# Kernel tuning notes

Measured on AMD Instinct MI355X. Metric: run time of the kernel, lower is better.

The kernel has to match this reference:

```python
import jax, jax.numpy as jnp
import numpy as np
from itertools import product

N_CODONS = 2
ORDER = 2
N_STATES = 25          # calc_number_of_states() with nCodons=2
ALPHA6 = 6             # alphabet_size + 2
OFFSET = 8 + 3 * N_CODONS       # 14, first insert state
TERM1 = OFFSET + 3 * (N_CODONS + 1)  # 23, terminal_1 state

CODE = {'A': [0], 'C': [1], 'G': [2], 'T': [3], 'N': [0, 1, 2, 3], 'X': [5]}


def _state_entries(state, emissions, x_must_preceed):
    ems = ['N'] * (ORDER - len(emissions) + 1) + list(emissions)[-(ORDER + 1):]
    allowed = [[state]]
    for i, e in enumerate(ems):
        allowed.append(CODE[e] + ([4] if i < ORDER - x_must_preceed else []))
    out = []
    for x in product(*allowed):
        found, ok = False, True
        for i in range(1, ORDER + 1):
            if found and x[i] == 4:
                ok = False
                break
            if x[i] != 4:
                found = True
        if ok:
            out.append(x)
    return out


def _emission_index_spec():
    entries, k = [], 0
    def add(state, ems, xp, trainable=True):
        nonlocal k
        ids = _state_entries(state, ems, xp)
        for t, x in enumerate(ids):
            entries.append((x, k + t if trainable else -1))
        if trainable:
            k += len(ids)
    add(0, 'N', 0); add(1, 'A', 0); add(2, 'AT', 0); add(3, 'ATG', 0, False)
    add(4, 'ATGN', 0); add(5, 'ATGNN', 0)
    for s in range(6, 6 + N_CODONS * 3 - 2):
        add(s, 'N', 0)
    add(4 + 3 * N_CODONS, 'T', ORDER)
    add(5 + 3 * N_CODONS, 'TA', ORDER); add(5 + 3 * N_CODONS, 'TG', ORDER)
    add(6 + 3 * N_CODONS, 'TAA', ORDER, False)
    add(6 + 3 * N_CODONS, 'TAG', ORDER, False)
    add(6 + 3 * N_CODONS, 'TGA', ORDER, False)
    add(7 + 3 * N_CODONS, 'N', ORDER)
    for s in range(8 + 3 * N_CODONS, 8 + 3 * N_CODONS + 3 * (N_CODONS + 1)):
        add(s, 'N', 0)
    for i in range(1, ORDER + 1):
        add(TERM1, 'X' * i, ORDER)
    add(TERM1 + 1, 'X' * (ORDER + 1), ORDER, False)
    idx = np.array([e[0] for e in entries], dtype=np.int32)
    widx = np.array([e[1] for e in entries], dtype=np.int32)
    return idx, widx

EM_IDX, EM_WIDX = _emission_index_spec()


def build_A(w):
    # sparse transition structure -> row-softmax over nonzeros -> dense [25,25]
    idx, vals = [], []
    def add(i, j, v):
        idx.append((i, j)); vals.append(v)
    n, k = N_CODONS, 0
    add(0, 0, 1 - w[k]); add(0, 1, w[k]); k += 1
    add(1, 2, 1.0); add(2, 3, 1.0)
    for i in range(n):
        add(3 + 3 * i, 4 + 3 * i, w[k + i])
    k += n
    for i in range(n):
        add(4 + 3 * i, 5 + 3 * i, 1.0)
    for i in range(n):
        add(5 + 3 * i, 6 + 3 * i, 1.0)
    for i in range(n + 1):
        add(3 + 3 * i, OFFSET + 3 * i, w[k + i])
    k += n + 1
    add(3 + 3 * n, 4 + 3 * n, 1 - w[k - 1])
    for i in range(n + 1):
        add(OFFSET + 3 * i, OFFSET + 1 + 3 * i, 1.0)
    for i in range(n + 1):
        add(OFFSET + 1 + 3 * i, OFFSET + 2 + 3 * i, 1.0)
    for i in range(n + 1):
        add(OFFSET + 2 + 3 * i, 4 + 3 * i, w[k + i])
    for i in range(n + 1):
        add(OFFSET + 2 + 3 * i, OFFSET + 3 * i, 1 - w[k + i])
    k += n + 1
    i_del = [3 + 3 * i for i in range(n) for _ in range(n - i)]
    j_del = [4 + 3 * j for i in range(1, n + 1) for j in range(i, n + 1)]
    for i, j in zip(i_del, j_del):
        add(i, j, 1 - w[k] * w[k] ** ((j - i) // 3))
    k += 1
    add(4 + 3 * n, 5 + 3 * n, 1.0); add(5 + 3 * n, 6 + 3 * n, 1.0)
    add(6 + 3 * n, 7 + 3 * n, 1.0)
    add(7 + 3 * n, 7 + 3 * n, 1.0); add(7 + 3 * n, TERM1, 1.0)
    add(TERM1, TERM1, 1.0); add(TERM1, TERM1 + 1, 1.0)
    add(TERM1 + 1, TERM1 + 1, 1.0)
    rows = np.array([i for i, _ in idx]); cols = np.array([j for _, j in idx])
    logits = jnp.stack([jnp.asarray(v, jnp.float32) for v in vals])
    M = jnp.full((N_STATES, N_STATES), -jnp.inf, jnp.float32).at[rows, cols].set(logits)
    A = jax.nn.softmax(M, axis=-1)
    return jnp.where(jnp.isfinite(M), A, 0.0)


def build_B(w):
    # sparse emission values (trainable weights or fixed 1), per-state softmax over nonzeros
    vals = jnp.where(EM_WIDX >= 0, w[np.clip(EM_WIDX, 0, None)], 1.0)
    rows = EM_IDX[:, 0]
    flat = EM_IDX[:, 1] * 36 + EM_IDX[:, 2] * 6 + EM_IDX[:, 3]
    M = jnp.full((N_STATES, ALPHA6 ** 3), -jnp.inf, jnp.float32).at[rows, flat].set(vals)
    B = jax.nn.softmax(M, axis=-1)
    return jnp.where(jnp.isfinite(M), B, 0.0)  # [25, 216]


def build_I(w):
    n_init = 3 + 3 * N_CODONS  # states 0..8 get initial mass
    p = jax.nn.softmax(w[:n_init])
    return jnp.zeros((N_STATES,), jnp.float32).at[:n_init].set(p)


def _forward(transition_kernel, emission_kernel, init_kernel, tokens):
    A = build_A(transition_kernel)
    Bf = build_B(emission_kernel)
    I = build_I(init_kernel)
    Bt, T = tokens.shape
    pad = jnp.full((Bt, ORDER), 4, tokens.dtype)  # '4' = no preceding emission
    tp = jnp.concatenate([pad, tokens], axis=1)
    flat = tp[:, :-2] * 36 + tp[:, 1:-1] * 6 + tp[:, 2:]  # [Bt, T]
    E = jnp.moveaxis(Bf.T[flat], 1, 0)  # [T, Bt, 25]
    alpha = I[None, :] * E[0]
    s = alpha.sum(-1, keepdims=True)
    alpha = alpha / s
    ll = jnp.log(s[..., 0])
    def step(carry, e):
        a, ll = carry
        a = (a @ A) * e
        s = a.sum(-1, keepdims=True)
        return (a / s, ll + jnp.log(s[..., 0])), None
    (alpha, ll), _ = jax.lax.scan(step, (alpha, ll), E[1:])
    return ll  # [Bt] per-sequence log-likelihood


def setup_inputs() -> dict:
    key = jax.random.key(0)
    k1, k2, k3, k4 = jax.random.split(key, 4)
    return {
        'transition_kernel': jax.random.normal(k1, (10,), jnp.float32) * 0.05,
        'emission_kernel': jax.random.normal(k2, (5400,), jnp.float32) * 0.05,
        'init_kernel': jax.random.normal(k3, (25,), jnp.float32) * 0.05,
        'tokens': jax.random.randint(k4, (512, 2048), 0, 4, jnp.int32),
    }


def reference(transition_kernel, emission_kernel, init_kernel, tokens):
    return _forward(transition_kernel, emission_kernel, init_kernel, tokens)
```

## Files before the change

### kernel.cpp

```cpp
#include <hip/hip_runtime.h>
#include <hip/hip_bf16.h>
#include <math.h>


typedef float v2f __attribute__((ext_vector_type(2)));
typedef float v4f __attribute__((ext_vector_type(4)));

#define NSTATES 25
#define NLIVE   23
#define NFLAT   216
#define NPACK   100
#define TLEN    2048
#define NSEQ    512
#define CHUNKS  16
#define CLEN    128

#define LOG16 2.772588722239781f

__device__ __constant__ int PERMC[24] = {1,4,2,5,3,6,7,10,8,11,9,12,
                                         14,17,15,18,16,19,20,0,21,13,22,23};
__device__ __constant__ int POSA[NLIVE] = {19,0,2,4,1,3,5,6,8,10,7,9,11,21,
                                           12,14,16,13,15,17,18,20,22};

struct WMap { short m[NSTATES * NFLAT]; };

constexpr WMap make_wmap() {
  WMap w{};
  for (int i = 0; i < NSTATES * NFLAT; i++) w.m[i] = -2;
  const unsigned char ST[29] = {0,1,2,3,4,5,6,7,8,9,10,11,11,12,12,12,13,
                                14,15,16,17,18,19,20,21,22,23,23,24};
  const unsigned char M1[29] = {0x1F,0x1F,0x1F,0x11,0x18,0x14,0x1F,0x1F,0x1F,
                                0x1F,0x0F,0x0F,0x0F,0x08,0x08,0x08,0x0F,
                                0x1F,0x1F,0x1F,0x1F,0x1F,0x1F,0x1F,0x1F,0x1F,
                                0x0F,0x0F,0x20};
  const unsigned char M2[29] = {0x1F,0x1F,0x11,0x18,0x14,0x1F,0x1F,0x1F,0x1F,
                                0x1F,0x0F,0x08,0x08,0x01,0x01,0x04,0x0F,
                                0x1F,0x1F,0x1F,0x1F,0x1F,0x1F,0x1F,0x1F,0x1F,
                                0x0F,0x20,0x20};
  const unsigned char M3[29] = {0x0F,0x01,0x08,0x04,0x0F,0x0F,0x0F,0x0F,0x0F,
                                0x0F,0x08,0x01,0x04,0x01,0x04,0x01,0x0F,
                                0x0F,0x0F,0x0F,0x0F,0x0F,0x0F,0x0F,0x0F,0x0F,
                                0x20,0x20,0x20};
  const unsigned char TR[29] = {1,1,1,0,1,1,1,1,1,1,1,1,1,0,0,0,1,
                                1,1,1,1,1,1,1,1,1,1,1,0};
  int k = 0;
  for (int s = 0; s < 29; s++) {
    for (int c1 = 0; c1 < 6; c1++) {
      if (!((M1[s] >> c1) & 1)) continue;
      for (int c2 = 0; c2 < 6; c2++) {
        if (!((M2[s] >> c2) & 1)) continue;
        if (c1 != 4 && c2 == 4) continue;
        for (int c3 = 0; c3 < 6; c3++) {
          if (!((M3[s] >> c3) & 1)) continue;
          w.m[ST[s] * NFLAT + c1 * 36 + c2 * 6 + c3] =
              TR[s] ? (short)(k++) : (short)-1;
        }
      }
    }
  }
  return w;
}
__device__ __constant__ WMap WMAP = make_wmap();

__device__ __forceinline__ unsigned short f2bf(float x) {
  unsigned int u = __float_as_uint(x);
  u += 0x7fffu + ((u >> 16) & 1u);
  return (unsigned short)(u >> 16);
}

struct Wp {
  v2f w01, wA, wB, wC, wD, wE, wF;
  float w4, w5, w8, w11;
};

__device__ __forceinline__ void step_pk(v2f (&Q)[12], const v4f (&F)[6],
                                        const Wp& W) {
  float a0 = Q[9].y,  a3 = Q[2].x,  a6 = Q[2].y,  a9 = Q[5].x;
  float a12 = Q[5].y, a13 = Q[10].y, a16 = Q[8].x, a19 = Q[8].y, a22 = Q[11].x;
  float q9x = Q[9].x, q10x = Q[10].x;

  v2f t01 = a0 * W.w01;
  v2f t44 = a3 * W.wA + a16 * W.wB;
  v2f t77 = a6 * W.wC + a19 * W.wD;
  float n7  = fmaf(a3, W.w4, t77.x);
  v2f tAA = a9 * W.wE + a22 * W.wF;
  float n10 = fmaf(a3, W.w5, fmaf(a6, W.w8, tAA.x));
  float n13 = fmaf(a13, W.w11, a12);

  v2f nQ1 = Q[0] * __builtin_shufflevector(F[0], F[0], 2, 3);
  v2f nQ2 = Q[1] * __builtin_shufflevector(F[1], F[1], 0, 1);
  v2f nQ4 = Q[3] * __builtin_shufflevector(F[2], F[2], 0, 1);
  v2f nQ5 = Q[4] * __builtin_shufflevector(F[2], F[2], 2, 3);
  v2f nQ7 = Q[6] * __builtin_shufflevector(F[3], F[3], 2, 3);
  v2f nQ8 = Q[7] * __builtin_shufflevector(F[4], F[4], 0, 1);

  Q[0]  = (v2f){ t01.y * F[0].x, t44.x * F[0].y };
  Q[3]  = (v2f){ n7    * F[1].z, n10   * F[1].w };
  Q[6]  = (v2f){ t44.y * F[3].x, t77.y * F[3].y };
  Q[9]  = (v2f){ tAA.y * F[4].z, t01.x * F[4].w };
  Q[10] = (v2f){ q9x   * F[5].x, n13   * F[5].y };
  Q[11].x = q10x * F[5].z;
  Q[1] = nQ1; Q[2] = nQ2; Q[4] = nQ4; Q[5] = nQ5; Q[7] = nQ7; Q[8] = nQ8;
}

__device__ __forceinline__ void renorm_pk(v2f (&Q)[12], float& L) {
  v2f acc = ((Q[0] + Q[1]) + (Q[2] + Q[3])) + ((Q[4] + Q[5]) + (Q[6] + Q[7]))
          + ((Q[8] + Q[9]) + (Q[10] + Q[11]));
  float s = acc.x + acc.y;
  if (s > 0.0f) {
    L += __logf(s);
    float r = __fdividef(1.0f, s);
    #pragma unroll
    for (int k = 0; k < 12; k++) Q[k] *= r;
  } else {
    L = -3.0e38f;
  }
}

#define LDROW(F, nt_) { int nt = (nt_); \
  const v4f* er = (const v4f*)(sBt + (((c12 << 2) + nt) << 5)); \
  F[0] = er[0]; F[1] = er[1]; F[2] = er[2]; \
  F[3] = er[3]; F[4] = er[4]; F[5] = er[5]; \
  c12 = p2 * 5 + nt; p2 = nt; }
#define LDSTEP(Fn, Fc, nt_) { LDROW(Fn, nt_); step_pk(Q, Fc, W); }

__global__ __launch_bounds__(512)
void hmm_kernel(const float* __restrict__ wT, const float* __restrict__ wE,
                const float* __restrict__ wI, const int* __restrict__ tokens,
                float* __restrict__ out) {
  __shared__ __align__(16) float          sBt[NPACK * 32];
  __shared__ __align__(16) unsigned short sT[CHUNKS * NLIVE * 24];
  __shared__ float sL[CHUNKS * NLIVE];
  __shared__ float sAW[24];
  __shared__ float sI[32];

  const int tid   = threadIdx.x;
  const int seq   = blockIdx.x;
  const int chunk = tid >> 5;
  const int row   = tid & 31;
  const int* trow = tokens + (size_t)seq * TLEN;

  for (int st = chunk; st < NLIVE; st += 16) {
    const int pos = POSA[st];
    float part = 0.0f;
    for (int c = row; c < NFLAT; c += 32) {
      short m = WMAP.m[st * NFLAT + c];
      if (m == -1) part += expf(1.0f);
      else if (m >= 0) part += expf(wE[m]);
    }
    #pragma unroll
    for (int m = 1; m < 32; m <<= 1) part += __shfl_xor(part, m, 32);
    float inv = 16.0f / part;
    for (int i = row; i < NPACK; i += 32) {
      int c12 = i >> 2, nt = i & 3;
      int p1 = c12 / 5, p2v = c12 - 5 * p1;
      int flat = p1 * 36 + p2v * 6 + nt;
      short m = WMAP.m[st * NFLAT + flat];
      float v = 0.0f;
      if (m == -1) v = expf(1.0f);
      else if (m >= 0) v = expf(wE[m]);
      sBt[i * 32 + pos] = v * inv;
    }
  }
  for (int i = tid; i < NPACK; i += 512) sBt[i * 32 + 23] = 0.0f;
  if (tid == 480) {
    const float w0 = wT[0], w1 = wT[1], w2 = wT[2], w3 = wT[3], w4 = wT[4];
    const float w5 = wT[5], w6 = wT[6], w7 = wT[7], w8 = wT[8], w9 = wT[9];
    { float e0 = expf(1.0f - w0), e1 = expf(w0), is = 1.0f / (e0 + e1);
      sAW[0] = e0 * is; sAW[1] = e1 * is; }
    { float e4 = expf(w1), e14 = expf(w3);
      float e7 = expf(1.0f - w9 * w9), e10 = expf(1.0f - w9 * w9 * w9);
      float is = 1.0f / (e4 + e14 + e7 + e10);
      sAW[2] = e4 * is;  sAW[3] = e14 * is;
      sAW[4] = e7 * is;  sAW[5] = e10 * is; }
    { float e7 = expf(w2), e17 = expf(w4), e10 = expf(1.0f - w9 * w9);
      float is = 1.0f / (e7 + e17 + e10);
      sAW[6] = e7 * is; sAW[7] = e17 * is; sAW[8] = e10 * is; }
    { float e20 = expf(w5), e10 = expf(1.0f - w5), is = 1.0f / (e20 + e10);
      sAW[9] = e20 * is; sAW[10] = e10 * is; }
    sAW[11] = 0.5f; sAW[12] = 0.5f;
    { float e4 = expf(w6), e14 = expf(1.0f - w6), is = 1.0f / (e4 + e14);
      sAW[13] = e4 * is; sAW[14] = e14 * is; }
    { float e7 = expf(w7), e17 = expf(1.0f - w7), is = 1.0f / (e7 + e17);
      sAW[15] = e7 * is; sAW[16] = e17 * is; }
    { float e10 = expf(w8), e20 = expf(1.0f - w8), is = 1.0f / (e10 + e20);
      sAW[17] = e10 * is; sAW[18] = e20 * is; }
    sAW[19] = 0.5f; sAW[20] = 0.5f;
  } else if (tid == 481) {
    float e[9], s = 0.0f;
    for (int i = 0; i < 9; i++) { e[i] = expf(wI[i]); s += e[i]; }
    float inv = 1.0f / s;
    for (int i = 0; i < 9; i++) sI[i] = e[i] * inv;
    for (int i = 9; i < 32; i++) sI[i] = 0.0f;
  }
  __syncthreads();

  float w[21];
  #pragma unroll
  for (int i = 0; i < 21; i++)
    w[i] = __uint_as_float(
        (unsigned)__builtin_amdgcn_readfirstlane(__float_as_uint(sAW[i])));
  Wp W;
  W.w01 = (v2f){w[0],  w[1]};
  W.wA  = (v2f){w[2],  w[3]};
  W.wB  = (v2f){w[13], w[14]};
  W.wC  = (v2f){w[6],  w[7]};
  W.wD  = (v2f){w[15], w[16]};
  W.wE  = (v2f){w[10], w[9]};
  W.wF  = (v2f){w[17], w[18]};
  W.w4 = w[4]; W.w5 = w[5]; W.w8 = w[8]; W.w11 = w[11];

  const int t0 = chunk * CLEN;

  v2f Q[12];
  #pragma unroll
  for (int k = 0; k < 12; k++) {
    Q[k].x = (row == PERMC[2 * k]) ? 1.0f : 0.0f;
    Q[k].y = (row == PERMC[2 * k + 1]) ? 1.0f : 0.0f;
  }
  float L = 0.0f;

  v4f FA[6], FB[6];
  int c12, p2;
  int4 q0 = *(const int4*)(trow + t0);
  int4 q1 = *(const int4*)(trow + t0 + 4);

  int b = 0;
  if (chunk == 0) {
    c12 = 20 + q0.x; p2 = q0.x;
    LDROW(FA, q0.y);
    LDSTEP(FB, FA, q0.z);
    LDSTEP(FA, FB, q0.w);
    LDSTEP(FB, FA, q1.x);
    LDSTEP(FA, FB, q1.y);
    LDSTEP(FB, FA, q1.z);
    LDSTEP(FA, FB, q1.w);
    step_pk(Q, FA, W);
    b = 1;
    q0 = *(const int4*)(trow + 8);
    q1 = *(const int4*)(trow + 12);
  } else {
    int2 pp = *(const int2*)(trow + t0 - 2);
    c12 = pp.x * 5 + pp.y; p2 = pp.y;
  }

  for (; b < CLEN / 8; b++) {
    int4 n0 = q0, n1 = q1;
    if (b + 1 < CLEN / 8) {
      n0 = *(const int4*)(trow + t0 + (b + 1) * 8);
      n1 = *(const int4*)(trow + t0 + (b + 1) * 8 + 4);
    }
    LDROW(FA, q0.x);
    LDSTEP(FB, FA, q0.y);
    LDSTEP(FA, FB, q0.z);
    LDSTEP(FB, FA, q0.w);
    LDSTEP(FA, FB, q1.x);
    LDSTEP(FB, FA, q1.y);
    LDSTEP(FA, FB, q1.z);
    LDSTEP(FB, FA, q1.w);
    step_pk(Q, FB, W);
    if (b & 1) renorm_pk(Q, L);
    q0 = n0; q1 = n1;
  }

  if (L > -1.0e38f) L -= (chunk == 0 ? 127.0f : 128.0f) * LOG16;

  if (row < NLIVE) {
    const int base = (chunk * NLIVE + row) * 24;
    #pragma unroll
    for (int k = 0; k < 12; k++) {
      ushort2 p; p.x = f2bf(Q[k].x); p.y = f2bf(Q[k].y);
      *(ushort2*)&sT[base + 2 * k] = p;
    }
    sL[chunk * NLIVE + row] = L;
  }
  __syncthreads();

  if (tid < 64) {
    const int lane = tid;
    const bool act = (lane < NLIVE);

    int jp = 23;
    #pragma unroll
    for (int pos = 0; pos < 23; pos++)
      if (PERMC[pos] == lane) jp = pos;

    const int tok0 = trow[0];
    const int idx0 = 96 + tok0;

    float v = act ? sI[lane] * sBt[idx0 * 32 + jp] : 0.0f;
    float s = v;
    #pragma unroll
    for (int m = 1; m < 32; m <<= 1) s += __shfl_xor(s, m, 32);
    float ll = __logf(s) - LOG16;
    v = act ? v * __fdividef(1.0f, s) : 0.0f;

    for (int c = 0; c < CHUNKS; c++) {
      float Lj  = act ? sL[c * NLIVE + lane] : -3.0e38f;
      float key = (act && v > 0.0f) ? Lj : -3.0e38f;
      float mx = key;
      #pragma unroll
      for (int m = 1; m < 32; m <<= 1) mx = fmaxf(mx, __shfl_xor(mx, m, 32));
      float wgt = (act && v > 0.0f) ? v * __expf(Lj - mx) : 0.0f;

      float nv = 0.0f;
      #pragma unroll
      for (int r = 0; r < NLIVE; r++) {
        float wr = __shfl(wgt, r, 64);
        nv += wr * __uint_as_float(((unsigned)sT[(c * NLIVE + r) * 24 + jp]) << 16);
      }
      float nva = act ? nv : 0.0f;
      float s2 = nva;
      #pragma unroll
      for (int m = 1; m < 32; m <<= 1) s2 += __shfl_xor(s2, m, 32);
      ll += mx + __logf(s2);
      v = act ? nv * __fdividef(1.0f, s2) : 0.0f;
    }

    if (lane == 0) out[seq] = ll;
  }
}

extern "C" void kernel_launch(void* const* d_in, const int* in_sizes, int n_in,
                              void* d_out, int out_size, void* d_ws, size_t ws_size,
                              hipStream_t stream) {
  const float* wT = (const float*)d_in[0];
  const float* wE = (const float*)d_in[1];
  const float* wI = (const float*)d_in[2];
  const int* tokens = (const int*)d_in[3];
  float* out = (float*)d_out;
  (void)d_ws; (void)ws_size;

  hmm_kernel<<<NSEQ, 512, 0, stream>>>(wT, wE, wI, tokens, out);
}
```

Baseline: 120.9 us.

## Precompute emission table once and stream rows via scalar loads per wavefront

Moves the per-block emission table construction into a separate prep kernel that writes a compact global table, removing redundant exp work from every block. The main loop now fetches each emission row with s_load_dwordx8 into scalar registers, using readfirstlane'd tokens and software double-buffering, instead of LDS vector reads. Blocks grow to 1024 threads with one 64-lane wave per chunk. Risks include scalar-cache latency on the serial dependency chain, half-idle 64-wide waves (only 23 lanes live), and the extra kernel launch.

Measured after the change: 148.6 us. 22.9% more time.

```diff
diff --git a/kernel.cpp b/kernel.cpp
--- a/kernel.cpp
+++ b/kernel.cpp
@@ -4,7 +4,7 @@
 
 
 typedef float v2f __attribute__((ext_vector_type(2)));
-typedef float v4f __attribute__((ext_vector_type(4)));
+typedef float v8f __attribute__((ext_vector_type(8)));
 
 #define NSTATES 25
 #define NLIVE   23
@@ -17,10 +17,16 @@
 
 #define LOG16 2.772588722239781f
 
+#define RFL(x) __builtin_amdgcn_readfirstlane(x)
+
 __device__ __constant__ int PERMC[24] = {1,4,2,5,3,6,7,10,8,11,9,12,
                                          14,17,15,18,16,19,20,0,21,13,22,23};
 __device__ __constant__ int POSA[NLIVE] = {19,0,2,4,1,3,5,6,8,10,7,9,11,21,
                                            12,14,16,13,15,17,18,20,22};
+__device__ __constant__ int SLOTP[24] = {12,13,0,1,2,3,14,15,4,5,6,7,
+                                         16,17,8,9,10,11,18,19,20,21,22,23};
+
+__device__ __align__(16) float gBt[NPACK * 24];
 
 struct WMap { short m[NSTATES * NFLAT]; };
 
@@ -73,8 +79,9 @@
   float w4, w5, w8, w11;
 };
 
-__device__ __forceinline__ void step_pk(v2f (&Q)[12], const v4f (&F)[6],
-                                        const Wp& W) {
+__device__ __forceinline__ void step_pk_s(v2f (&Q)[12], const v8f& A0,
+                                          const v8f& A1, const v8f& A2,
+                                          const Wp& W) {
   float a0 = Q[9].y,  a3 = Q[2].x,  a6 = Q[2].y,  a9 = Q[5].x;
   float a12 = Q[5].y, a13 = Q[10].y, a16 = Q[8].x, a19 = Q[8].y, a22 = Q[11].x;
   float q9x = Q[9].x, q10x = Q[10].x;
@@ -87,19 +94,19 @@
   float n10 = fmaf(a3, W.w5, fmaf(a6, W.w8, tAA.x));
   float n13 = fmaf(a13, W.w11, a12);
 
-  v2f nQ1 = Q[0] * __builtin_shufflevector(F[0], F[0], 2, 3);
-  v2f nQ2 = Q[1] * __builtin_shufflevector(F[1], F[1], 0, 1);
-  v2f nQ4 = Q[3] * __builtin_shufflevector(F[2], F[2], 0, 1);
-  v2f nQ5 = Q[4] * __builtin_shufflevector(F[2], F[2], 2, 3);
-  v2f nQ7 = Q[6] * __builtin_shufflevector(F[3], F[3], 2, 3);
-  v2f nQ8 = Q[7] * __builtin_shufflevector(F[4], F[4], 0, 1);
-
-  Q[0]  = (v2f){ t01.y * F[0].x, t44.x * F[0].y };
-  Q[3]  = (v2f){ n7    * F[1].z, n10   * F[1].w };
-  Q[6]  = (v2f){ t44.y * F[3].x, t77.y * F[3].y };
-  Q[9]  = (v2f){ tAA.y * F[4].z, t01.x * F[4].w };
-  Q[10] = (v2f){ q9x   * F[5].x, n13   * F[5].y };
-  Q[11].x = q10x * F[5].z;
+  v2f nQ1 = Q[0] * (v2f){A0[0], A0[1]};
+  v2f nQ2 = Q[1] * (v2f){A0[2], A0[3]};
+  v2f nQ4 = Q[3] * (v2f){A0[4], A0[5]};
+  v2f nQ5 = Q[4] * (v2f){A0[6], A0[7]};
+  v2f nQ7 = Q[6] * (v2f){A1[0], A1[1]};
+  v2f nQ8 = Q[7] * (v2f){A1[2], A1[3]};
+
+  Q[0]  = (v2f){t01.y, t44.x} * (v2f){A1[4], A1[5]};
+  Q[3]  = (v2f){n7,    n10  } * (v2f){A1[6], A1[7]};
+  Q[6]  = (v2f){t44.y, t77.y} * (v2f){A2[0], A2[1]};
+  Q[9]  = (v2f){tAA.y, t01.x} * (v2f){A2[2], A2[3]};
+  Q[10] = (v2f){q9x,   n13  } * (v2f){A2[4], A2[5]};
+  Q[11].x = q10x * A2[6];
   Q[1] = nQ1; Q[2] = nQ2; Q[4] = nQ4; Q[5] = nQ5; Q[7] = nQ7; Q[8] = nQ8;
 }
 
@@ -117,18 +124,56 @@
   }
 }
 
-#define LDROW(F, nt_) { int nt = (nt_); \
-  const v4f* er = (const v4f*)(sBt + (((c12 << 2) + nt) << 5)); \
-  F[0] = er[0]; F[1] = er[1]; F[2] = er[2]; \
-  F[3] = er[3]; F[4] = er[4]; F[5] = er[5]; \
+#define ISSUE_ROW(R0, R1, R2, nt_) { int nt = (nt_); \
+  unsigned long long p_ = gb + (unsigned long long)((((c12 << 2) + nt) * 96)); \
+  asm volatile("s_load_dwordx8 %0, %3, 0x0\n\t" \
+               "s_load_dwordx8 %1, %3, 0x20\n\t" \
+               "s_load_dwordx8 %2, %3, 0x40" \
+               : "=&s"(R0), "=&s"(R1), "=&s"(R2) : "s"(p_)); \
   c12 = p2 * 5 + nt; p2 = nt; }
-#define LDSTEP(Fn, Fc, nt_) { LDROW(Fn, nt_); step_pk(Q, Fc, W); }
-
-__global__ __launch_bounds__(512)
+
+#define ROWWAIT(R0, R1, R2) \
+  asm volatile("s_waitcnt lgkmcnt(0)" : "+s"(R0), "+s"(R1), "+s"(R2))
+
+#define SSTEP(C0, C1, C2, N0, N1, N2, nt_) { \
+  ROWWAIT(C0, C1, C2); \
+  ISSUE_ROW(N0, N1, N2, nt_); \
+  step_pk_s(Q, C0, C1, C2, W); }
+
+__global__ __launch_bounds__(32)
+void prep_kernel(const float* __restrict__ wE) {
+  const int st  = blockIdx.x;
+  const int row = threadIdx.x;
+  const int pos = POSA[st];
+  const int slot = SLOTP[pos];
+  float part = 0.0f;
+  for (int c = row; c < NFLAT; c += 32) {
+    short m = WMAP.m[st * NFLAT + c];
+    if (m == -1) part += expf(1.0f);
+    else if (m >= 0) part += expf(wE[m]);
+  }
+  #pragma unroll
+  for (int m = 1; m < 32; m <<= 1) part += __shfl_xor(part, m, 32);
+  float inv = 16.0f / part;
+  for (int i = row; i < NPACK; i += 32) {
+    int c12 = i >> 2, nt = i & 3;
+    int p1 = c12 / 5, p2v = c12 - 5 * p1;
+    int flat = p1 * 36 + p2v * 6 + nt;
+    short m = WMAP.m[st * NFLAT + flat];
+    float v = 0.0f;
+    if (m == -1) v = expf(1.0f);
+    else if (m >= 0) v = expf(wE[m]);
+    gBt[i * 24 + slot] = v * inv;
+  }
+  if (st == 0) {
+    for (int i = row; i < NPACK; i += 32) gBt[i * 24 + 23] = 0.0f;
+  }
+}
+
+__global__ __launch_bounds__(1024)
 void hmm_kernel(const float* __restrict__ wT, const float* __restrict__ wE,
                 const float* __restrict__ wI, const int* __restrict__ tokens,
                 float* __restrict__ out) {
-  __shared__ __align__(16) float          sBt[NPACK * 32];
   __shared__ __align__(16) unsigned short sT[CHUNKS * NLIVE * 24];
   __shared__ float sL[CHUNKS * NLIVE];
   __shared__ float sAW[24];
@@ -136,33 +181,10 @@
 
   const int tid   = threadIdx.x;
   const int seq   = blockIdx.x;
-  const int chunk = tid >> 5;
-  const int row   = tid & 31;
+  const int lane  = tid & 63;
+  const int chunk = RFL(tid >> 6);
   const int* trow = tokens + (size_t)seq * TLEN;
 
-  for (int st = chunk; st < NLIVE; st += 16) {
-    const int pos = POSA[st];
-    float part = 0.0f;
-    for (int c = row; c < NFLAT; c += 32) {
-      short m = WMAP.m[st * NFLAT + c];
-      if (m == -1) part += expf(1.0f);
-      else if (m >= 0) part += expf(wE[m]);
-    }
-    #pragma unroll
-    for (int m = 1; m < 32; m <<= 1) part += __shfl_xor(part, m, 32);
-    float inv = 16.0f / part;
-    for (int i = row; i < NPACK; i += 32) {
-      int c12 = i >> 2, nt = i & 3;
-      int p1 = c12 / 5, p2v = c12 - 5 * p1;
-      int flat = p1 * 36 + p2v * 6 + nt;
-      short m = WMAP.m[st * NFLAT + flat];
-      float v = 0.0f;
-      if (m == -1) v = expf(1.0f);
-      else if (m >= 0) v = expf(wE[m]);
-      sBt[i * 32 + pos] = v * inv;
-    }
-  }
-  for (int i = tid; i < NPACK; i += 512) sBt[i * 32 + 23] = 0.0f;
   if (tid == 480) {
     const float w0 = wT[0], w1 = wT[1], w2 = wT[2], w3 = wT[3], w4 = wT[4];
     const float w5 = wT[5], w6 = wT[6], w7 = wT[7], w8 = wT[8], w9 = wT[9];
@@ -211,84 +233,106 @@
   W.w4 = w[4]; W.w5 = w[5]; W.w8 = w[8]; W.w11 = w[11];
 
   const int t0 = chunk * CLEN;
+  const unsigned long long gb = (unsigned long long)(const void*)gBt;
 
   v2f Q[12];
   #pragma unroll
   for (int k = 0; k < 12; k++) {
-    Q[k].x = (row == PERMC[2 * k]) ? 1.0f : 0.0f;
-    Q[k].y = (row == PERMC[2 * k + 1]) ? 1.0f : 0.0f;
+    Q[k].x = (lane == PERMC[2 * k]) ? 1.0f : 0.0f;
+    Q[k].y = (lane == PERMC[2 * k + 1]) ? 1.0f : 0.0f;
   }
   float L = 0.0f;
 
-  v4f FA[6], FB[6];
+  v8f A0, A1, A2, B0, B1, B2;
   int c12, p2;
   int4 q0 = *(const int4*)(trow + t0);
   int4 q1 = *(const int4*)(trow + t0 + 4);
 
-  int b = 0;
+  int b;
   if (chunk == 0) {
-    c12 = 20 + q0.x; p2 = q0.x;
-    LDROW(FA, q0.y);
-    LDSTEP(FB, FA, q0.z);
-    LDSTEP(FA, FB, q0.w);
-    LDSTEP(FB, FA, q1.x);
-    LDSTEP(FA, FB, q1.y);
-    LDSTEP(FB, FA, q1.z);
-    LDSTEP(FA, FB, q1.w);
-    step_pk(Q, FA, W);
+    int s0 = RFL(q0.x), s1 = RFL(q0.y), s2 = RFL(q0.z), s3 = RFL(q0.w);
+    int s4 = RFL(q1.x), s5 = RFL(q1.y), s6 = RFL(q1.z), s7 = RFL(q1.w);
+    int4 nq0 = *(const int4*)(trow + 8);
+    int4 nq1 = *(const int4*)(trow + 12);
+    int sn0 = RFL(nq0.x);
+    c12 = 20 + s0; p2 = s0;
+    ISSUE_ROW(B0, B1, B2, s1);
+    SSTEP(B0, B1, B2, A0, A1, A2, s2);
+    SSTEP(A0, A1, A2, B0, B1, B2, s3);
+    SSTEP(B0, B1, B2, A0, A1, A2, s4);
+    SSTEP(A0, A1, A2, B0, B1, B2, s5);
+    SSTEP(B0, B1, B2, A0, A1, A2, s6);
+    SSTEP(A0, A1, A2, B0, B1, B2, s7);
+    SSTEP(B0, B1, B2, A0, A1, A2, sn0);
     b = 1;
-    q0 = *(const int4*)(trow + 8);
-    q1 = *(const int4*)(trow + 12);
+    q0 = nq0; q1 = nq1;
   } else {
     int2 pp = *(const int2*)(trow + t0 - 2);
-    c12 = pp.x * 5 + pp.y; p2 = pp.y;
-  }
-
-  for (; b < CLEN / 8; b++) {
-    int4 n0 = q0, n1 = q1;
-    if (b + 1 < CLEN / 8) {
-      n0 = *(const int4*)(trow + t0 + (b + 1) * 8);
-      n1 = *(const int4*)(trow + t0 + (b + 1) * 8 + 4);
-    }
-    LDROW(FA, q0.x);
-    LDSTEP(FB, FA, q0.y);
-    LDSTEP(FA, FB, q0.z);
-    LDSTEP(FB, FA, q0.w);
-    LDSTEP(FA, FB, q1.x);
-    LDSTEP(FB, FA, q1.y);
-    LDSTEP(FA, FB, q1.z);
-    LDSTEP(FB, FA, q1.w);
-    step_pk(Q, FB, W);
+    int sp0 = RFL(pp.x), sp1 = RFL(pp.y);
+    int s0 = RFL(q0.x);
+    c12 = sp0 * 5 + sp1; p2 = sp1;
+    ISSUE_ROW(A0, A1, A2, s0);
+    b = 0;
+  }
+
+  for (; b < CLEN / 8 - 1; b++) {
+    int4 n0 = *(const int4*)(trow + t0 + (b + 1) * 8);
+    int4 n1 = *(const int4*)(trow + t0 + (b + 1) * 8 + 4);
+    int s1 = RFL(q0.y), s2 = RFL(q0.z), s3 = RFL(q0.w);
+    int s4 = RFL(q1.x), s5 = RFL(q1.y), s6 = RFL(q1.z), s7 = RFL(q1.w);
+    int sn0 = RFL(n0.x);
+    SSTEP(A0, A1, A2, B0, B1, B2, s1);
+    SSTEP(B0, B1, B2, A0, A1, A2, s2);
+    SSTEP(A0, A1, A2, B0, B1, B2, s3);
+    SSTEP(B0, B1, B2, A0, A1, A2, s4);
+    SSTEP(A0, A1, A2, B0, B1, B2, s5);
+    SSTEP(B0, B1, B2, A0, A1, A2, s6);
+    SSTEP(A0, A1, A2, B0, B1, B2, s7);
+    SSTEP(B0, B1, B2, A0, A1, A2, sn0);
     if (b & 1) renorm_pk(Q, L);
     q0 = n0; q1 = n1;
   }
+  {
+    int s1 = RFL(q0.y), s2 = RFL(q0.z), s3 = RFL(q0.w);
+    int s4 = RFL(q1.x), s5 = RFL(q1.y), s6 = RFL(q1.z), s7 = RFL(q1.w);
+    SSTEP(A0, A1, A2, B0, B1, B2, s1);
+    SSTEP(B0, B1, B2, A0, A1, A2, s2);
+    SSTEP(A0, A1, A2, B0, B1, B2, s3);
+    SSTEP(B0, B1, B2, A0, A1, A2, s4);
+    SSTEP(A0, A1, A2, B0, B1, B2, s5);
+    SSTEP(B0, B1, B2, A0, A1, A2, s6);
+    SSTEP(A0, A1, A2, B0, B1, B2, s7);
+    ROWWAIT(B0, B1, B2);
+    step_pk_s(Q, B0, B1, B2, W);
+    renorm_pk(Q, L);
+  }
 
   if (L > -1.0e38f) L -= (chunk == 0 ? 127.0f : 128.0f) * LOG16;
 
-  if (row < NLIVE) {
-    const int base = (chunk * NLIVE + row) * 24;
+  if (lane < NLIVE) {
+    const int base = (chunk * NLIVE + lane) * 24;
     #pragma unroll
     for (int k = 0; k < 12; k++) {
       ushort2 p; p.x = f2bf(Q[k].x); p.y = f2bf(Q[k].y);
       *(ushort2*)&sT[base + 2 * k] = p;
     }
-    sL[chunk * NLIVE + row] = L;
+    sL[chunk * NLIVE + lane] = L;
   }
   __syncthreads();
 
   if (tid < 64) {
-    const int lane = tid;
-    const bool act = (lane < NLIVE);
+    const int lane0 = tid;
+    const bool act = (lane0 < NLIVE);
 
     int jp = 23;
     #pragma unroll
     for (int pos = 0; pos < 23; pos++)
-      if (PERMC[pos] == lane) jp = pos;
+      if (PERMC[pos] == lane0) jp = pos;
 
     const int tok0 = trow[0];
     const int idx0 = 96 + tok0;
 
-    float v = act ? sI[lane] * sBt[idx0 * 32 + jp] : 0.0f;
+    float v = act ? sI[lane0] * gBt[idx0 * 24 + SLOTP[jp]] : 0.0f;
     float s = v;
     #pragma unroll
     for (int m = 1; m < 32; m <<= 1) s += __shfl_xor(s, m, 32);
@@ -296,7 +340,7 @@
     v = act ? v * __fdividef(1.0f, s) : 0.0f;
 
     for (int c = 0; c < CHUNKS; c++) {
-      float Lj  = act ? sL[c * NLIVE + lane] : -3.0e38f;
+      float Lj  = act ? sL[c * NLIVE + lane0] : -3.0e38f;
       float key = (act && v > 0.0f) ? Lj : -3.0e38f;
       float mx = key;
       #pragma unroll
@@ -317,7 +361,7 @@
       v = act ? nv * __fdividef(1.0f, s2) : 0.0f;
     }
 
-    if (lane == 0) out[seq] = ll;
+    if (lane0 == 0) out[seq] = ll;
   }
 }
 
@@ -331,5 +375,6 @@
   float* out = (float*)d_out;
   (void)d_ws; (void)ws_size;
 
-  hmm_kernel<<<NSEQ, 512, 0, stream>>>(wT, wE, wI, tokens, out);
-}
+  prep_kernel<<<NLIVE, 32, 0, stream>>>(wE);
+  hmm_kernel<<<NSEQ, 1024, 0, stream>>>(wT, wE, wI, tokens, out);
+}
```

## Pack two transfer-matrix rows per thread and halve block size

Applied to the files above, without the earlier changes.

Each thread now carries two rows of the chunked transfer matrix (row16 and row16+16) as the x/y lanes of packed float2 vectors, instead of one row split across packed state pairs. The block shrinks from 512 to 256 threads and the emission table pitch drops from 32 to 28 floats. The aim is to amortize the shared-memory emission row loads over two rows and drop the 9 idle lanes per 32-lane group. In exchange each thread does twice the arithmetic and holds more registers, and fewer threads per block may reduce latency hiding.

Result: no change. 122.2 us (+1.0%).

```diff
diff --git a/kernel.cpp b/kernel.cpp
--- a/kernel.cpp
+++ b/kernel.cpp
@@ -10,6 +10,7 @@
 #define NLIVE   23
 #define NFLAT   216
 #define NPACK   100
+#define PITCH   28
 #define TLEN    2048
 #define NSEQ    512
 #define CHUNKS  16
@@ -68,67 +69,88 @@
   return (unsigned short)(u >> 16);
 }
 
-struct Wp {
-  v2f w01, wA, wB, wC, wD, wE, wF;
+struct Wp2 {
+  v2f w0, w1, w2, w3, w6, w7, w9, w10, w13, w14, w15, w16, w17, w18;
   float w4, w5, w8, w11;
 };
 
-__device__ __forceinline__ void step_pk(v2f (&Q)[12], const v4f (&F)[6],
-                                        const Wp& W) {
-  float a0 = Q[9].y,  a3 = Q[2].x,  a6 = Q[2].y,  a9 = Q[5].x;
-  float a12 = Q[5].y, a13 = Q[10].y, a16 = Q[8].x, a19 = Q[8].y, a22 = Q[11].x;
-  float q9x = Q[9].x, q10x = Q[10].x;
-
-  v2f t01 = a0 * W.w01;
-  v2f t44 = a3 * W.wA + a16 * W.wB;
-  v2f t77 = a6 * W.wC + a19 * W.wD;
-  float n7  = fmaf(a3, W.w4, t77.x);
-  v2f tAA = a9 * W.wE + a22 * W.wF;
-  float n10 = fmaf(a3, W.w5, fmaf(a6, W.w8, tAA.x));
-  float n13 = fmaf(a13, W.w11, a12);
-
-  v2f nQ1 = Q[0] * __builtin_shufflevector(F[0], F[0], 2, 3);
-  v2f nQ2 = Q[1] * __builtin_shufflevector(F[1], F[1], 0, 1);
-  v2f nQ4 = Q[3] * __builtin_shufflevector(F[2], F[2], 0, 1);
-  v2f nQ5 = Q[4] * __builtin_shufflevector(F[2], F[2], 2, 3);
-  v2f nQ7 = Q[6] * __builtin_shufflevector(F[3], F[3], 2, 3);
-  v2f nQ8 = Q[7] * __builtin_shufflevector(F[4], F[4], 0, 1);
-
-  Q[0]  = (v2f){ t01.y * F[0].x, t44.x * F[0].y };
-  Q[3]  = (v2f){ n7    * F[1].z, n10   * F[1].w };
-  Q[6]  = (v2f){ t44.y * F[3].x, t77.y * F[3].y };
-  Q[9]  = (v2f){ tAA.y * F[4].z, t01.x * F[4].w };
-  Q[10] = (v2f){ q9x   * F[5].x, n13   * F[5].y };
-  Q[11].x = q10x * F[5].z;
-  Q[1] = nQ1; Q[2] = nQ2; Q[4] = nQ4; Q[5] = nQ5; Q[7] = nQ7; Q[8] = nQ8;
-}
-
-__device__ __forceinline__ void renorm_pk(v2f (&Q)[12], float& L) {
-  v2f acc = ((Q[0] + Q[1]) + (Q[2] + Q[3])) + ((Q[4] + Q[5]) + (Q[6] + Q[7]))
-          + ((Q[8] + Q[9]) + (Q[10] + Q[11]));
-  float s = acc.x + acc.y;
-  if (s > 0.0f) {
-    L += __logf(s);
-    float r = __fdividef(1.0f, s);
-    #pragma unroll
-    for (int k = 0; k < 12; k++) Q[k] *= r;
-  } else {
-    L = -3.0e38f;
-  }
+#define SP(x) ((v2f){(x), (x)})
+#define FMA2(a, ws, c) ((v2f){fmaf((a).x, (ws), (c).x), \
+                              fmaf((a).y, (ws), (c).y)})
+
+__device__ __forceinline__ void step_pk2(v2f (&Q)[23], const v4f (&F)[6],
+                                         const Wp2& W) {
+  v2f o19 = Q[19], o4 = Q[4], o5 = Q[5], o10 = Q[10], o11 = Q[11];
+  v2f o21 = Q[21], o16 = Q[16], o17 = Q[17], o22 = Q[22];
+  v2f o18 = Q[18], o20 = Q[20];
+
+  v2f n0  = o19 * W.w0;
+  v2f n1  = o19 * W.w1;
+  v2f n4  = o4 * W.w2  + o16 * W.w13;
+  v2f n14 = o4 * W.w3  + o16 * W.w14;
+  v2f t77 = o5 * W.w6  + o17 * W.w15;
+  v2f n7  = FMA2(o4, W.w4, t77);
+  v2f n17 = o5 * W.w7  + o17 * W.w16;
+  v2f tAA = o10 * W.w10 + o22 * W.w17;
+  v2f n10 = FMA2(o4, W.w5, FMA2(o5, W.w8, tAA));
+  v2f n20 = o10 * W.w9 + o22 * W.w18;
+  v2f n13 = FMA2(o21, W.w11, o11);
+
+  v2f s2  = Q[0]  * SP(F[0].z),  s3  = Q[1]  * SP(F[0].w);
+  v2f s4  = Q[2]  * SP(F[1].x),  s5  = Q[3]  * SP(F[1].y);
+  v2f s8  = Q[6]  * SP(F[2].x),  s9  = Q[7]  * SP(F[2].y);
+  v2f s10 = Q[8]  * SP(F[2].z),  s11 = Q[9]  * SP(F[2].w);
+  v2f s14 = Q[12] * SP(F[3].z),  s15 = Q[13] * SP(F[3].w);
+  v2f s16 = Q[14] * SP(F[4].x),  s17 = Q[15] * SP(F[4].y);
+  v2f s20 = o18 * SP(F[5].x);
+  v2f s22 = o20 * SP(F[5].z);
+
+  Q[0]  = n1  * SP(F[0].x);
+  Q[1]  = n4  * SP(F[0].y);
+  Q[6]  = n7  * SP(F[1].z);
+  Q[7]  = n10 * SP(F[1].w);
+  Q[12] = n14 * SP(F[3].x);
+  Q[13] = n17 * SP(F[3].y);
+  Q[18] = n20 * SP(F[4].z);
+  Q[19] = n0  * SP(F[4].w);
+  Q[20] = s20;
+  Q[21] = n13 * SP(F[5].y);
+  Q[22] = s22;
+  Q[2] = s2;  Q[3] = s3;  Q[4] = s4;  Q[5] = s5;
+  Q[8] = s8;  Q[9] = s9;  Q[10] = s10; Q[11] = s11;
+  Q[14] = s14; Q[15] = s15; Q[16] = s16; Q[17] = s17;
+}
+
+__device__ __forceinline__ void renorm_pk2(v2f (&Q)[23], v2f& L) {
+  v2f ax = (((Q[0] + Q[2]) + (Q[4] + Q[6])) +
+            ((Q[8] + Q[10]) + (Q[12] + Q[14]))) +
+           ((Q[16] + Q[18]) + (Q[20] + Q[22]));
+  v2f ay = (((Q[1] + Q[3]) + (Q[5] + Q[7])) +
+            ((Q[9] + Q[11]) + (Q[13] + Q[15]))) +
+           ((Q[17] + Q[19]) + Q[21]);
+  v2f s = ax + ay;
+  bool okA = s.x > 0.0f, okB = s.y > 0.0f;
+  L.x = okA ? L.x + __logf(s.x) : -3.0e38f;
+  L.y = okB ? L.y + __logf(s.y) : -3.0e38f;
+  v2f r;
+  r.x = okA ? __fdividef(1.0f, s.x) : 1.0f;
+  r.y = okB ? __fdividef(1.0f, s.y) : 1.0f;
+  #pragma unroll
+  for (int k = 0; k < 23; k++) Q[k] *= r;
 }
 
 #define LDROW(F, nt_) { int nt = (nt_); \
-  const v4f* er = (const v4f*)(sBt + (((c12 << 2) + nt) << 5)); \
+  const v4f* er = (const v4f*)(sBt + (((c12 << 2) + nt) * PITCH)); \
   F[0] = er[0]; F[1] = er[1]; F[2] = er[2]; \
   F[3] = er[3]; F[4] = er[4]; F[5] = er[5]; \
   c12 = p2 * 5 + nt; p2 = nt; }
-#define LDSTEP(Fn, Fc, nt_) { LDROW(Fn, nt_); step_pk(Q, Fc, W); }
-
-__global__ __launch_bounds__(512)
+#define LDSTEP(Fn, Fc, nt_) { LDROW(Fn, nt_); step_pk2(Q, Fc, W); }
+
+__global__ __launch_bounds__(256)
 void hmm_kernel(const float* __restrict__ wT, const float* __restrict__ wE,
                 const float* __restrict__ wI, const int* __restrict__ tokens,
                 float* __restrict__ out) {
-  __shared__ __align__(16) float          sBt[NPACK * 32];
+  __shared__ __align__(16) float          sBt[NPACK * PITCH];
   __shared__ __align__(16) unsigned short sT[CHUNKS * NLIVE * 24];
   __shared__ float sL[CHUNKS * NLIVE];
   __shared__ float sAW[24];
@@ -136,34 +158,37 @@
 
   const int tid   = threadIdx.x;
   const int seq   = blockIdx.x;
-  const int chunk = tid >> 5;
-  const int row   = tid & 31;
+  const int chunk = tid >> 4;
+  const int row16 = tid & 15;
   const int* trow = tokens + (size_t)seq * TLEN;
 
-  for (int st = chunk; st < NLIVE; st += 16) {
-    const int pos = POSA[st];
-    float part = 0.0f;
-    for (int c = row; c < NFLAT; c += 32) {
-      short m = WMAP.m[st * NFLAT + c];
-      if (m == -1) part += expf(1.0f);
-      else if (m >= 0) part += expf(wE[m]);
-    }
-    #pragma unroll
-    for (int m = 1; m < 32; m <<= 1) part += __shfl_xor(part, m, 32);
-    float inv = 16.0f / part;
-    for (int i = row; i < NPACK; i += 32) {
-      int c12 = i >> 2, nt = i & 3;
-      int p1 = c12 / 5, p2v = c12 - 5 * p1;
-      int flat = p1 * 36 + p2v * 6 + nt;
-      short m = WMAP.m[st * NFLAT + flat];
-      float v = 0.0f;
-      if (m == -1) v = expf(1.0f);
-      else if (m >= 0) v = expf(wE[m]);
-      sBt[i * 32 + pos] = v * inv;
-    }
-  }
-  for (int i = tid; i < NPACK; i += 512) sBt[i * 32 + 23] = 0.0f;
-  if (tid == 480) {
+  {
+    const int g32 = tid >> 5, r32 = tid & 31;
+    for (int st = g32; st < NLIVE; st += 8) {
+      const int pos = POSA[st];
+      float part = 0.0f;
+      for (int c = r32; c < NFLAT; c += 32) {
+        short m = WMAP.m[st * NFLAT + c];
+        if (m == -1) part += expf(1.0f);
+        else if (m >= 0) part += expf(wE[m]);
+      }
+      #pragma unroll
+      for (int m = 1; m < 32; m <<= 1) part += __shfl_xor(part, m, 32);
+      float inv = 16.0f / part;
+      for (int i = r32; i < NPACK; i += 32) {
+        int c12 = i >> 2, nt = i & 3;
+        int p1 = c12 / 5, p2v = c12 - 5 * p1;
+        int flat = p1 * 36 + p2v * 6 + nt;
+        short m = WMAP.m[st * NFLAT + flat];
+        float v = 0.0f;
+        if (m == -1) v = expf(1.0f);
+        else if (m >= 0) v = expf(wE[m]);
+        sBt[i * PITCH + pos] = v * inv;
+      }
+    }
+  }
+  for (int i = tid; i < NPACK; i += 256) sBt[i * PITCH + 23] = 0.0f;
+  if (tid == 224) {
     const float w0 = wT[0], w1 = wT[1], w2 = wT[2], w3 = wT[3], w4 = wT[4];
     const float w5 = wT[5], w6 = wT[6], w7 = wT[7], w8 = wT[8], w9 = wT[9];
     { float e0 = expf(1.0f - w0), e1 = expf(w0), is = 1.0f / (e0 + e1);
@@ -186,7 +211,7 @@
     { float e10 = expf(w8), e20 = expf(1.0f - w8), is = 1.0f / (e10 + e20);
       sAW[17] = e10 * is; sAW[18] = e20 * is; }
     sAW[19] = 0.5f; sAW[20] = 0.5f;
-  } else if (tid == 481) {
+  } else if (tid == 225) {
     float e[9], s = 0.0f;
     for (int i = 0; i < 9; i++) { e[i] = expf(wI[i]); s += e[i]; }
     float inv = 1.0f / s;
@@ -200,25 +225,22 @@
   for (int i = 0; i < 21; i++)
     w[i] = __uint_as_float(
         (unsigned)__builtin_amdgcn_readfirstlane(__float_as_uint(sAW[i])));
-  Wp W;
-  W.w01 = (v2f){w[0],  w[1]};
-  W.wA  = (v2f){w[2],  w[3]};
-  W.wB  = (v2f){w[13], w[14]};
-  W.wC  = (v2f){w[6],  w[7]};
-  W.wD  = (v2f){w[15], w[16]};
-  W.wE  = (v2f){w[10], w[9]};
-  W.wF  = (v2f){w[17], w[18]};
+  Wp2 W;
+  W.w0 = SP(w[0]);   W.w1 = SP(w[1]);   W.w2 = SP(w[2]);   W.w3 = SP(w[3]);
+  W.w6 = SP(w[6]);   W.w7 = SP(w[7]);   W.w9 = SP(w[9]);   W.w10 = SP(w[10]);
+  W.w13 = SP(w[13]); W.w14 = SP(w[14]); W.w15 = SP(w[15]); W.w16 = SP(w[16]);
+  W.w17 = SP(w[17]); W.w18 = SP(w[18]);
   W.w4 = w[4]; W.w5 = w[5]; W.w8 = w[8]; W.w11 = w[11];
 
   const int t0 = chunk * CLEN;
 
-  v2f Q[12];
+  v2f Q[23];
   #pragma unroll
-  for (int k = 0; k < 12; k++) {
-    Q[k].x = (row == PERMC[2 * k]) ? 1.0f : 0.0f;
-    Q[k].y = (row == PERMC[2 * k + 1]) ? 1.0f : 0.0f;
-  }
-  float L = 0.0f;
+  for (int p = 0; p < 23; p++) {
+    Q[p].x = (row16 == PERMC[p]) ? 1.0f : 0.0f;
+    Q[p].y = (row16 + 16 == PERMC[p]) ? 1.0f : 0.0f;
+  }
+  v2f L = (v2f){0.0f, 0.0f};
 
   v4f FA[6], FB[6];
   int c12, p2;
@@ -235,7 +257,7 @@
     LDSTEP(FA, FB, q1.y);
     LDSTEP(FB, FA, q1.z);
     LDSTEP(FA, FB, q1.w);
-    step_pk(Q, FA, W);
+    step_pk2(Q, FA, W);
     b = 1;
     q0 = *(const int4*)(trow + 8);
     q1 = *(const int4*)(trow + 12);
@@ -258,21 +280,36 @@
     LDSTEP(FB, FA, q1.y);
     LDSTEP(FA, FB, q1.z);
     LDSTEP(FB, FA, q1.w);
-    step_pk(Q, FB, W);
-    if (b & 1) renorm_pk(Q, L);
+    step_pk2(Q, FB, W);
+    if (b & 1) renorm_pk2(Q, L);
     q0 = n0; q1 = n1;
   }
 
-  if (L > -1.0e38f) L -= (chunk == 0 ? 127.0f : 128.0f) * LOG16;
-
-  if (row < NLIVE) {
-    const int base = (chunk * NLIVE + row) * 24;
+  const float undo = (chunk == 0 ? 127.0f : 128.0f) * LOG16;
+  if (L.x > -1.0e38f) L.x -= undo;
+  if (L.y > -1.0e38f) L.y -= undo;
+
+  {
+    const int baseA = (chunk * NLIVE + row16) * 24;
     #pragma unroll
     for (int k = 0; k < 12; k++) {
-      ushort2 p; p.x = f2bf(Q[k].x); p.y = f2bf(Q[k].y);
-      *(ushort2*)&sT[base + 2 * k] = p;
-    }
-    sL[chunk * NLIVE + row] = L;
+      ushort2 p;
+      p.x = f2bf(Q[2 * k].x);
+      p.y = (2 * k + 1 < 23) ? f2bf(Q[2 * k + 1].x) : (unsigned short)0;
+      *(ushort2*)&sT[baseA + 2 * k] = p;
+    }
+    sL[chunk * NLIVE + row16] = L.x;
+    if (row16 < 7) {
+      const int baseB = (chunk * NLIVE + row16 + 16) * 24;
+      #pragma unroll
+      for (int k = 0; k < 12; k++) {
+        ushort2 p;
+        p.x = f2bf(Q[2 * k].y);
+        p.y = (2 * k + 1 < 23) ? f2bf(Q[2 * k + 1].y) : (unsigned short)0;
+        *(ushort2*)&sT[baseB + 2 * k] = p;
+      }
+      sL[chunk * NLIVE + row16 + 16] = L.y;
+    }
   }
   __syncthreads();
 
@@ -288,7 +325,7 @@
     const int tok0 = trow[0];
     const int idx0 = 96 + tok0;
 
-    float v = act ? sI[lane] * sBt[idx0 * 32 + jp] : 0.0f;
+    float v = act ? sI[lane] * sBt[idx0 * PITCH + jp] : 0.0f;
     float s = v;
     #pragma unroll
     for (int m = 1; m < 32; m <<= 1) s += __shfl_xor(s, m, 32);
@@ -331,5 +368,5 @@
   float* out = (float*)d_out;
   (void)d_ws; (void)ws_size;
 
-  hmm_kernel<<<NSEQ, 512, 0, stream>>>(wT, wE, wI, tokens, out);
-}
+  hmm_kernel<<<NSEQ, 256, 0, stream>>>(wT, wE, wI, tokens, out);
+}
```
